# Optimization experiments

Hardware: AMD Instinct MI355X
Metric: run time of the kernel (lower is better)

## Reference

```python
import jax, jax.numpy as jnp
import numpy as np

B, C_IN, L, NCLASS = 256, 6, 512, 10

def setup_inputs() -> dict:
    key = jax.random.key(0)
    ks = jax.random.split(key, 16)
    g = lambda k, shp, s=0.05: jax.random.normal(k, shp, dtype=jnp.float32) * s
    return {
        "x": jax.random.normal(ks[0], (B, C_IN, L), dtype=jnp.float32),
        "conv1_w": g(ks[1], (32, C_IN, 3)),
        "conv1_b": g(ks[2], (32,)),
        "bn1_g": jnp.ones((32,), jnp.float32),
        "bn1_b": jnp.zeros((32,), jnp.float32),
        "bn1_m": g(ks[3], (32,)),
        "bn1_v": jnp.abs(g(ks[4], (32,))) + 1.0,
        "conv2_w": g(ks[5], (64, 32, 3)),
        "conv2_b": g(ks[6], (64,)),
        "bn2_g": jnp.ones((64,), jnp.float32),
        "bn2_b": jnp.zeros((64,), jnp.float32),
        "bn2_m": g(ks[7], (64,)),
        "bn2_v": jnp.abs(g(ks[8], (64,))) + 1.0,
        "wq": g(ks[9], (64, 64)),
        "bq": g(ks[10], (64,)),
        "wk": g(ks[11], (64, 64)),
        "bk": g(ks[12], (64,)),
        "wv": g(ks[13], (64, 64)),
        "bv": g(ks[14], (64,)),
        "fc_w": g(ks[15], (NCLASS, 64)),
        "fc_b": jnp.zeros((NCLASS,), jnp.float32),
    }

def _conv1d(x, w, b):
    # x: [B, C, L], w: [O, C, 3], padding=1 -> same length
    y = jax.lax.conv_general_dilated(
        x, w, window_strides=(1,), padding=[(1, 1)],
        dimension_numbers=("NCH", "OIH", "NCH"))
    return y + b[None, :, None]

def _bn(x, g, b, m, v, eps=1e-5):
    # eval-mode BatchNorm1d over channel dim of [B, C, L]
    inv = g * jax.lax.rsqrt(v + eps)
    return x * inv[None, :, None] + (b - m * inv)[None, :, None]

def reference(x, conv1_w, conv1_b, bn1_g, bn1_b, bn1_m, bn1_v,
              conv2_w, conv2_b, bn2_g, bn2_b, bn2_m, bn2_v,
              wq, bq, wk, bk, wv, bv, fc_w, fc_b):
    h = jax.nn.relu(_bn(_conv1d(x, conv1_w, conv1_b), bn1_g, bn1_b, bn1_m, bn1_v))
    h = jax.nn.relu(_bn(_conv1d(h, conv2_w, conv2_b), bn2_g, bn2_b, bn2_m, bn2_v))
    h = h.transpose(0, 2, 1)                      # [B, L, 64]
    q = h @ wq.T + bq
    k = h @ wk.T + bk
    v = h @ wv.T + bv
    scores = jnp.einsum("bqd,bkd->bqk", q, k) / jnp.sqrt(jnp.float32(64.0))
    attn = jax.nn.softmax(scores, axis=-1)
    out = jnp.einsum("bqk,bkd->bqd", attn, v)     # [B, L, 64]
    pooled = out.mean(axis=1)                     # [B, 64]
    return pooled @ fc_w.T + fc_b                 # [B, n_class]
```

## Files before the change

kernel.cpp:

```cpp
#include <hip/hip_runtime.h>
#include <hip/hip_bf16.h>


#define NB 256
#define LL 512
#define CIN 6
#define NCLASS 10
#define SLAB 9472
#define QSC 0.18033688f

typedef __bf16 bf16x8 __attribute__((ext_vector_type(8)));
typedef float f32x4 __attribute__((ext_vector_type(4)));
typedef unsigned short us4 __attribute__((ext_vector_type(4)));

static __device__ __forceinline__ unsigned short f2b(float f) {
    __bf16 h = (__bf16)f;
    return __builtin_bit_cast(unsigned short, h);
}

__global__ __launch_bounds__(256) void prep_weights(
    const float* __restrict__ w1, const float* __restrict__ cb1,
    const float* __restrict__ g1, const float* __restrict__ be1,
    const float* __restrict__ m1, const float* __restrict__ v1,
    const float* __restrict__ w2, const float* __restrict__ cb2,
    const float* __restrict__ g2, const float* __restrict__ be2,
    const float* __restrict__ m2, const float* __restrict__ v2,
    const float* __restrict__ wq, const float* __restrict__ wk,
    const float* __restrict__ wv,
    unsigned short* __restrict__ w1p, float* __restrict__ b1f,
    unsigned short* __restrict__ w2p, float* __restrict__ b2f,
    unsigned short* __restrict__ wqp, unsigned short* __restrict__ wkp,
    unsigned short* __restrict__ wvp)
{
    const int t = threadIdx.x;
    for (int idx = t; idx < 1024; idx += 256) {
        int c = idx >> 5, k = idx & 31;
        int dl = k >> 3, ci = k & 7;
        float inv = g1[c] * rsqrtf(v1[c] + 1e-5f);
        float val = (dl < 3 && ci < 6) ? w1[c * 18 + ci * 3 + dl] * inv : 0.f;
        w1p[idx] = f2b(val);
    }
    if (t < 32) {
        float inv = g1[t] * rsqrtf(v1[t] + 1e-5f);
        b1f[t] = be1[t] + (cb1[t] - m1[t]) * inv;
    }
    for (int idx = t; idx < 2048; idx += 256) {
        int c2 = idx >> 5, ci = idx & 31;
        float inv = g2[c2] * rsqrtf(v2[c2] + 1e-5f);
        const float* wp = w2 + c2 * 96 + ci * 3;
        w2p[c2 * 96 +      ci] = f2b(wp[0] * inv);
        w2p[c2 * 96 + 32 + ci] = f2b(wp[1] * inv);
        w2p[c2 * 96 + 64 + ci] = f2b(wp[2] * inv);
    }
    if (t >= 64 && t < 128) {
        int c2 = t - 64;
        float inv = g2[c2] * rsqrtf(v2[c2] + 1e-5f);
        b2f[c2] = be2[c2] + (cb2[c2] - m2[c2]) * inv;
    }
    for (int idx = t; idx < 4096; idx += 256) {
        wqp[idx] = f2b(wq[idx] * QSC);
        wkp[idx] = f2b(wk[idx]);
        wvp[idx] = f2b(wv[idx]);
    }
}

__global__ __launch_bounds__(1024, 4) void fused_all(
    const float* __restrict__ x,
    const unsigned short* __restrict__ w1p, const float* __restrict__ b1f,
    const unsigned short* __restrict__ w2p, const float* __restrict__ b2f,
    const unsigned short* __restrict__ wqp, const unsigned short* __restrict__ wkp,
    const unsigned short* __restrict__ wvp,
    const float* __restrict__ bq, const float* __restrict__ bk,
    const float* __restrict__ bvp,
    const float* __restrict__ fcw, const float* __restrict__ fcb,
    float* __restrict__ outp)
{
    const int b = blockIdx.x;
    const int t = threadIdx.x;
    const int w = t >> 6, lane = t & 63, quad = lane >> 4, lc = lane & 15;

    __shared__ __align__(16) char smem[16 * SLAB + 6144];
    char* myslab = smem + w * SLAB;
    unsigned short* h1sl = (unsigned short*)(myslab + 3072);
    unsigned short* Ts   = (unsigned short*)(myslab + 4608);
    unsigned short* Kf   = (unsigned short*)myslab;
    unsigned short* Vf   = (unsigned short*)(myslab + 4096);
    float* redw   = (float*)(myslab + 8192);
    float* pooled = (float*)(smem + 8448);
    unsigned short* xstage = (unsigned short*)(smem + 16 * SLAB);

    if (t < 768) {
        int ci = t >> 7, j4 = (t & 127) * 4;
        float4 xv = *(const float4*)(x + ((size_t)b * CIN + ci) * LL + j4);
        us4 pk;
        pk[0] = f2b(xv.x); pk[1] = f2b(xv.y); pk[2] = f2b(xv.z); pk[3] = f2b(xv.w);
        *(us4*)&xstage[ci * 512 + j4] = pk;
    }
    __syncthreads();

    bf16x8 bW1[2];
    #pragma unroll
    for (int nt = 0; nt < 2; nt++)
        bW1[nt] = *(const bf16x8*)(w1p + (nt * 16 + lc) * 32 + quad * 8);
    float b1v[2] = {b1f[lc], b1f[16 + lc]};
    f32x4 h1acc[3][2];
    #pragma unroll
    for (int mt = 0; mt < 3; mt++) {
        int pos = w * 32 - 2 + mt * 16 + lc + quad;
        bool ok = (quad < 3) && (pos >= 0) && (pos < LL);
        int posc = pos < 0 ? 0 : (pos > 511 ? 511 : pos);
        bf16x8 aX;
        #pragma unroll
        for (int u = 0; u < 6; u++) {
            __bf16 vb = __builtin_bit_cast(__bf16, xstage[u * 512 + posc]);
            aX[u] = ok ? vb : (__bf16)0.f;
        }
        aX[6] = (__bf16)0.f; aX[7] = (__bf16)0.f;
        #pragma unroll
        for (int nt = 0; nt < 2; nt++) {
            f32x4 z = {0.f, 0.f, 0.f, 0.f};
            h1acc[mt][nt] = __builtin_amdgcn_mfma_f32_16x16x32_bf16(aX, bW1[nt], z, 0, 0, 0);
        }
    }
    #pragma unroll
    for (int mt = 0; mt < 3; mt++)
        #pragma unroll
        for (int nt = 0; nt < 2; nt++)
            #pragma unroll
            for (int r = 0; r < 4; r++) {
                int j = mt * 16 + quad * 4 + r;
                if (j < 34) {
                    int pos = w * 32 - 1 + j;
                    float y = h1acc[mt][nt][r] + b1v[nt];
                    y = (pos >= 0 && pos < LL && y > 0.f) ? y : 0.f;
                    h1sl[j * 40 + nt * 16 + lc] = f2b(y);
                }
            }

    bf16x8 bX[2][3], aW2[4][3];
    #pragma unroll
    for (int rt = 0; rt < 2; rt++)
        #pragma unroll
        for (int kc = 0; kc < 3; kc++)
            bX[rt][kc] = *(const bf16x8*)&h1sl[(rt * 16 + lc + kc) * 40 + quad * 8];
    #pragma unroll
    for (int nt = 0; nt < 4; nt++)
        #pragma unroll
        for (int kc = 0; kc < 3; kc++)
            aW2[nt][kc] = *(const bf16x8*)(w2p + (nt * 16 + lc) * 96 + kc * 32 + quad * 8);

    f32x4 acc2[4][2];
    #pragma unroll
    for (int nt = 0; nt < 4; nt++)
        #pragma unroll
        for (int rt = 0; rt < 2; rt++) {
            f32x4 a = {0.f, 0.f, 0.f, 0.f};
            a = __builtin_amdgcn_mfma_f32_16x16x32_bf16(aW2[nt][0], bX[rt][0], a, 0, 0, 0);
            a = __builtin_amdgcn_mfma_f32_16x16x32_bf16(aW2[nt][1], bX[rt][1], a, 0, 0, 0);
            acc2[nt][rt] = __builtin_amdgcn_mfma_f32_16x16x32_bf16(aW2[nt][2], bX[rt][2], a, 0, 0, 0);
        }

    #pragma unroll
    for (int nt = 0; nt < 4; nt++) {
        const float4 bb2 = *(const float4*)&b2f[nt * 16 + quad * 4];
        #pragma unroll
        for (int rt = 0; rt < 2; rt++) {
            us4 pk;
            float y0 = acc2[nt][rt][0] + bb2.x; pk[0] = f2b(y0 > 0.f ? y0 : 0.f);
            float y1 = acc2[nt][rt][1] + bb2.y; pk[1] = f2b(y1 > 0.f ? y1 : 0.f);
            float y2 = acc2[nt][rt][2] + bb2.z; pk[2] = f2b(y2 > 0.f ? y2 : 0.f);
            float y3 = acc2[nt][rt][3] + bb2.w; pk[3] = f2b(y3 > 0.f ? y3 : 0.f);
            *(us4*)&Ts[(rt * 16 + lc) * 72 + nt * 16 + quad * 4] = pk;
        }
    }
    bf16x8 aH[2][2];
    #pragma unroll
    for (int rt = 0; rt < 2; rt++)
        #pragma unroll
        for (int kc = 0; kc < 2; kc++)
            aH[rt][kc] = *(const bf16x8*)&Ts[(rt * 16 + lc) * 72 + kc * 32 + quad * 8];

    bf16x8 aQ[2][2];
    for (int p = 0; p < 2; p++) {
        const unsigned short* wsrc = p ? wkp : wqp;
        const float* bsrc = p ? bk : bq;
        const float bscl = p ? 1.0f : QSC;
        #pragma unroll
        for (int nt = 0; nt < 4; nt++) {
            bf16x8 aW[2];
            #pragma unroll
            for (int kc = 0; kc < 2; kc++)
                aW[kc] = *(const bf16x8*)(wsrc + (nt * 16 + lc) * 64 + kc * 32 + quad * 8);
            float4 bb = *(const float4*)&bsrc[nt * 16 + quad * 4];
            bb.x *= bscl; bb.y *= bscl; bb.z *= bscl; bb.w *= bscl;
            #pragma unroll
            for (int rt = 0; rt < 2; rt++) {
                f32x4 a = {0.f, 0.f, 0.f, 0.f};
                a = __builtin_amdgcn_mfma_f32_16x16x32_bf16(aW[0], aH[rt][0], a, 0, 0, 0);
                a = __builtin_amdgcn_mfma_f32_16x16x32_bf16(aW[1], aH[rt][1], a, 0, 0, 0);
                us4 pk;
                pk[0] = f2b(a[0] + bb.x); pk[1] = f2b(a[1] + bb.y);
                pk[2] = f2b(a[2] + bb.z); pk[3] = f2b(a[3] + bb.w);
                *(us4*)&Ts[(rt * 16 + lc) * 72 + nt * 16 + quad * 4] = pk;
            }
        }
        #pragma unroll
        for (int rt = 0; rt < 2; rt++)
            #pragma unroll
            for (int kc = 0; kc < 2; kc++) {
                bf16x8 fr = *(const bf16x8*)&Ts[(rt * 16 + lc) * 72 + kc * 32 + quad * 8];
                if (p == 0) aQ[rt][kc] = fr;
                else *(bf16x8*)&Kf[((rt * 2 + kc) << 9) + lane * 8] = fr;
            }
    }

    #pragma unroll
    for (int nt = 0; nt < 4; nt++) {
        bf16x8 bW[2];
        #pragma unroll
        for (int kc = 0; kc < 2; kc++)
            bW[kc] = *(const bf16x8*)(wvp + (nt * 16 + lc) * 64 + kc * 32 + quad * 8);
        const float bvv = bvp[nt * 16 + lc];
        #pragma unroll
        for (int rt = 0; rt < 2; rt++) {
            f32x4 a = {0.f, 0.f, 0.f, 0.f};
            a = __builtin_amdgcn_mfma_f32_16x16x32_bf16(aH[rt][0], bW[0], a, 0, 0, 0);
            a = __builtin_amdgcn_mfma_f32_16x16x32_bf16(aH[rt][1], bW[1], a, 0, 0, 0);
            us4 pk;
            pk[0] = f2b(a[0] + bvv); pk[1] = f2b(a[1] + bvv);
            pk[2] = f2b(a[2] + bvv); pk[3] = f2b(a[3] + bvv);
            *(us4*)&Vf[nt * 512 + quad * 128 + lc * 8 + rt * 4] = pk;
        }
    }

    __syncthreads();

    f32x4 outacc[2][4];
    #pragma unroll
    for (int rt = 0; rt < 2; rt++)
        #pragma unroll
        for (int dt = 0; dt < 4; dt++) outacc[rt][dt] = (f32x4){0.f, 0.f, 0.f, 0.f};
    float den[2] = {0.f, 0.f};

    bf16x8 bK[2][2], bKn[2][2];
    {
        const unsigned short* sK = (const unsigned short*)smem;
        #pragma unroll
        for (int nt = 0; nt < 2; nt++)
            #pragma unroll
            for (int kc = 0; kc < 2; kc++)
                bK[nt][kc] = *(const bf16x8*)&sK[((nt * 2 + kc) << 9) + lane * 8];
    }

    for (int cc = 0; cc < 16; cc++) {
        f32x4 sv[2][2];
        #pragma unroll
        for (int nt = 0; nt < 2; nt++)
            #pragma unroll
            for (int rt = 0; rt < 2; rt++) {
                f32x4 z = {0.f, 0.f, 0.f, 0.f};
                z = __builtin_amdgcn_mfma_f32_16x16x32_bf16(bK[nt][0], aQ[rt][0], z, 0, 0, 0);
                sv[nt][rt] = __builtin_amdgcn_mfma_f32_16x16x32_bf16(bK[nt][1], aQ[rt][1], z, 0, 0, 0);
            }
        const unsigned short* sV = (const unsigned short*)(smem + cc * SLAB + 4096);
        bf16x8 bV[4];
        #pragma unroll
        for (int dt = 0; dt < 4; dt++)
            bV[dt] = *(const bf16x8*)&sV[dt * 512 + lane * 8];
        if (cc < 15) {
            const unsigned short* sKn = (const unsigned short*)(smem + (cc + 1) * SLAB);
            #pragma unroll
            for (int nt = 0; nt < 2; nt++)
                #pragma unroll
                for (int kc = 0; kc < 2; kc++)
                    bKn[nt][kc] = *(const bf16x8*)&sKn[((nt * 2 + kc) << 9) + lane * 8];
        }
        bf16x8 aP[2];
        #pragma unroll
        for (int rt = 0; rt < 2; rt++)
            #pragma unroll
            for (int nt = 0; nt < 2; nt++)
                #pragma unroll
                for (int reg = 0; reg < 4; reg++) {
                    float p = __builtin_amdgcn_exp2f(sv[nt][rt][reg]);
                    den[rt] += p;
                    aP[rt][nt * 4 + reg] = (__bf16)p;
                }
        #pragma unroll
        for (int dt = 0; dt < 4; dt++) {
            outacc[0][dt] = __builtin_amdgcn_mfma_f32_16x16x32_bf16(aP[0], bV[dt], outacc[0][dt], 0, 0, 0);
            outacc[1][dt] = __builtin_amdgcn_mfma_f32_16x16x32_bf16(aP[1], bV[dt], outacc[1][dt], 0, 0, 0);
        }
        #pragma unroll
        for (int nt = 0; nt < 2; nt++)
            #pragma unroll
            for (int kc = 0; kc < 2; kc++)
                bK[nt][kc] = bKn[nt][kc];
    }

    float rden[2][4];
    #pragma unroll
    for (int rt = 0; rt < 2; rt++) {
        float d2 = den[rt];
        d2 += __shfl_xor(d2, 16);
        d2 += __shfl_xor(d2, 32);
        d2 = 1.0f / d2;
        #pragma unroll
        for (int reg = 0; reg < 4; reg++)
            rden[rt][reg] = __shfl(d2, quad * 4 + reg);
    }
    #pragma unroll
    for (int dt = 0; dt < 4; dt++) {
        float ps = 0.f;
        #pragma unroll
        for (int rt = 0; rt < 2; rt++)
            #pragma unroll
            for (int reg = 0; reg < 4; reg++)
                ps += outacc[rt][dt][reg] * rden[rt][reg];
        ps += __shfl_xor(ps, 16);
        ps += __shfl_xor(ps, 32);
        if (quad == 0) redw[dt * 16 + lc] = ps;
    }
    __syncthreads();
    if (t < 64) {
        float s = 0.f;
        #pragma unroll
        for (int ww = 0; ww < 16; ww++)
            s += *(const float*)(smem + ww * SLAB + 8192 + t * 4);
        pooled[t] = s * (1.0f / 512.0f);
    }
    __syncthreads();
    if (t < NCLASS) {
        float acc = fcb[t];
        #pragma unroll
        for (int d = 0; d < 64; d++) acc += pooled[d] * fcw[t * 64 + d];
        outp[b * NCLASS + t] = acc;
    }
}

extern "C" void kernel_launch(void* const* d_in, const int* in_sizes, int n_in,
                              void* d_out, int out_size, void* d_ws, size_t ws_size,
                              hipStream_t stream)
{
    const float* x   = (const float*)d_in[0];
    const float* w1  = (const float*)d_in[1];
    const float* cb1 = (const float*)d_in[2];
    const float* g1  = (const float*)d_in[3];
    const float* be1 = (const float*)d_in[4];
    const float* m1  = (const float*)d_in[5];
    const float* v1  = (const float*)d_in[6];
    const float* w2  = (const float*)d_in[7];
    const float* cb2 = (const float*)d_in[8];
    const float* g2  = (const float*)d_in[9];
    const float* be2 = (const float*)d_in[10];
    const float* m2  = (const float*)d_in[11];
    const float* v2  = (const float*)d_in[12];
    const float* wq  = (const float*)d_in[13];
    const float* bq  = (const float*)d_in[14];
    const float* wk  = (const float*)d_in[15];
    const float* bk  = (const float*)d_in[16];
    const float* wv  = (const float*)d_in[17];
    const float* bv  = (const float*)d_in[18];
    const float* fcw = (const float*)d_in[19];
    const float* fcb = (const float*)d_in[20];
    float* out = (float*)d_out;

    char* ws = (char*)d_ws;
    unsigned short* w1p = (unsigned short*)(ws);
    float*          b1f = (float*)(ws + 2048u);
    float*          b2f = (float*)(ws + 2176u);
    unsigned short* w2p = (unsigned short*)(ws + 2432u);
    unsigned short* wqp = (unsigned short*)(ws + 14720u);
    unsigned short* wkp = (unsigned short*)(ws + 22912u);
    unsigned short* wvp = (unsigned short*)(ws + 31104u);

    prep_weights<<<dim3(1), 256, 0, stream>>>(w1, cb1, g1, be1, m1, v1,
                                              w2, cb2, g2, be2, m2, v2,
                                              wq, wk, wv,
                                              w1p, b1f, w2p, b2f, wqp, wkp, wvp);
    fused_all<<<dim3(NB), 1024, 0, stream>>>(x, w1p, b1f, w2p, b2f,
                                             wqp, wkp, wvp,
                                             bq, bk, bv, fcw, fcb, out);
}
```

Baseline: 130.8 us.

## Keep Q/K/H in registers via permuted weight layout and software-pipeline QK^T

Weights for Q/K/V are pre-permuted so MFMA output fragments map directly into the next MFMA's input layout, removing the LDS round-trips through the Ts scratch buffer. The per-wave slab is shrunk, x is staged position-major as 8-wide vectors so conv1 input is a single vector load, and conv1 results are written as packed vectors. The attention loop computes the next chunk's scores after the PV MFMAs under raised wave priority to overlap exp with matrix work. It adds register pressure and relies on an intricate channel permutation being correct.

```diff
diff --git a/kernel.cpp b/kernel.cpp
--- a/kernel.cpp
+++ b/kernel.cpp
@@ -6,12 +6,14 @@
 #define LL 512
 #define CIN 6
 #define NCLASS 10
-#define SLAB 9472
+#define SLAB 8192
 #define QSC 0.18033688f
 
 typedef __bf16 bf16x8 __attribute__((ext_vector_type(8)));
 typedef float f32x4 __attribute__((ext_vector_type(4)));
 typedef unsigned short us4 __attribute__((ext_vector_type(4)));
+typedef unsigned short us8 __attribute__((ext_vector_type(8)));
+typedef unsigned int u32x4 __attribute__((ext_vector_type(4)));
 
 static __device__ __forceinline__ unsigned short f2b(float f) {
     __bf16 h = (__bf16)f;
@@ -58,9 +60,12 @@
         b2f[c2] = be2[c2] + (cb2[c2] - m2[c2]) * inv;
     }
     for (int idx = t; idx < 4096; idx += 256) {
-        wqp[idx] = f2b(wq[idx] * QSC);
-        wkp[idx] = f2b(wk[idx]);
-        wvp[idx] = f2b(wv[idx]);
+        int d = idx >> 6, k = idx & 63;
+        int kc = k >> 5, quad = (k >> 3) & 3, e = k & 7;
+        int ch = kc * 32 + (e >> 2) * 16 + quad * 4 + (e & 3);
+        wqp[idx] = f2b(wq[d * 64 + ch] * QSC);
+        wkp[idx] = f2b(wk[d * 64 + ch]);
+        wvp[idx] = f2b(wv[d * 64 + ch]);
     }
 }
 
@@ -79,22 +84,22 @@
     const int t = threadIdx.x;
     const int w = t >> 6, lane = t & 63, quad = lane >> 4, lc = lane & 15;
 
-    __shared__ __align__(16) char smem[16 * SLAB + 6144];
+    __shared__ __align__(16) char smem[16 * SLAB + 8192];
     char* myslab = smem + w * SLAB;
-    unsigned short* h1sl = (unsigned short*)(myslab + 3072);
-    unsigned short* Ts   = (unsigned short*)(myslab + 4608);
+    unsigned short* h1sl = (unsigned short*)myslab;
     unsigned short* Kf   = (unsigned short*)myslab;
     unsigned short* Vf   = (unsigned short*)(myslab + 4096);
-    float* redw   = (float*)(myslab + 8192);
-    float* pooled = (float*)(smem + 8448);
     unsigned short* xstage = (unsigned short*)(smem + 16 * SLAB);
-
-    if (t < 768) {
-        int ci = t >> 7, j4 = (t & 127) * 4;
-        float4 xv = *(const float4*)(x + ((size_t)b * CIN + ci) * LL + j4);
-        us4 pk;
-        pk[0] = f2b(xv.x); pk[1] = f2b(xv.y); pk[2] = f2b(xv.z); pk[3] = f2b(xv.w);
-        *(us4*)&xstage[ci * 512 + j4] = pk;
+    float* redw   = (float*)(smem + 16 * SLAB) + w * 64;
+    float* pooled = (float*)(smem + 16 * SLAB + 4096);
+
+    if (t < 512) {
+        us8 pk;
+        #pragma unroll
+        for (int ci = 0; ci < 6; ci++)
+            pk[ci] = f2b(x[((size_t)b * CIN + ci) * LL + t]);
+        pk[6] = 0; pk[7] = 0;
+        *(us8*)&xstage[t * 8] = pk;
     }
     __syncthreads();
 
@@ -102,40 +107,36 @@
     #pragma unroll
     for (int nt = 0; nt < 2; nt++)
         bW1[nt] = *(const bf16x8*)(w1p + (nt * 16 + lc) * 32 + quad * 8);
-    float b1v[2] = {b1f[lc], b1f[16 + lc]};
-    f32x4 h1acc[3][2];
+    f32x4 b1q[2];
+    #pragma unroll
+    for (int nt = 0; nt < 2; nt++)
+        b1q[nt] = *(const f32x4*)&b1f[nt * 16 + quad * 4];
     #pragma unroll
     for (int mt = 0; mt < 3; mt++) {
-        int pos = w * 32 - 2 + mt * 16 + lc + quad;
-        bool ok = (quad < 3) && (pos >= 0) && (pos < LL);
-        int posc = pos < 0 ? 0 : (pos > 511 ? 511 : pos);
-        bf16x8 aX;
-        #pragma unroll
-        for (int u = 0; u < 6; u++) {
-            __bf16 vb = __builtin_bit_cast(__bf16, xstage[u * 512 + posc]);
-            aX[u] = ok ? vb : (__bf16)0.f;
-        }
-        aX[6] = (__bf16)0.f; aX[7] = (__bf16)0.f;
+        int j = mt * 16 + lc;
+        int P = w * 32 - 1 + j;
+        int src = P + quad - 1;
+        bool okx = (src >= 0) && (src < LL);
+        int srcc = src < 0 ? 0 : (src > 511 ? 511 : src);
+        u32x4 xv = *(const u32x4*)&xstage[srcc * 8];
+        if (!okx) { xv[0] = 0u; xv[1] = 0u; xv[2] = 0u; xv[3] = 0u; }
+        bf16x8 aX = __builtin_bit_cast(bf16x8, xv);
+        bool pv = (P >= 0) && (P < LL);
         #pragma unroll
         for (int nt = 0; nt < 2; nt++) {
             f32x4 z = {0.f, 0.f, 0.f, 0.f};
-            h1acc[mt][nt] = __builtin_amdgcn_mfma_f32_16x16x32_bf16(aX, bW1[nt], z, 0, 0, 0);
-        }
-    }
-    #pragma unroll
-    for (int mt = 0; mt < 3; mt++)
-        #pragma unroll
-        for (int nt = 0; nt < 2; nt++)
+            f32x4 h = __builtin_amdgcn_mfma_f32_16x16x32_bf16(bW1[nt], aX, z, 0, 0, 0);
+            us4 pk;
             #pragma unroll
             for (int r = 0; r < 4; r++) {
-                int j = mt * 16 + quad * 4 + r;
-                if (j < 34) {
-                    int pos = w * 32 - 1 + j;
-                    float y = h1acc[mt][nt][r] + b1v[nt];
-                    y = (pos >= 0 && pos < LL && y > 0.f) ? y : 0.f;
-                    h1sl[j * 40 + nt * 16 + lc] = f2b(y);
-                }
+                float y = h[r] + b1q[nt][r];
+                y = (pv && y > 0.f) ? y : 0.f;
+                pk[r] = f2b(y);
             }
+            if (j < 34)
+                *(us4*)&h1sl[j * 40 + nt * 16 + quad * 4] = pk;
+        }
+    }
 
     bf16x8 bX[2][3], aW2[4][3];
     #pragma unroll
@@ -160,77 +161,94 @@
             acc2[nt][rt] = __builtin_amdgcn_mfma_f32_16x16x32_bf16(aW2[nt][2], bX[rt][2], a, 0, 0, 0);
         }
 
-    #pragma unroll
-    for (int nt = 0; nt < 4; nt++) {
-        const float4 bb2 = *(const float4*)&b2f[nt * 16 + quad * 4];
-        #pragma unroll
-        for (int rt = 0; rt < 2; rt++) {
-            us4 pk;
-            float y0 = acc2[nt][rt][0] + bb2.x; pk[0] = f2b(y0 > 0.f ? y0 : 0.f);
-            float y1 = acc2[nt][rt][1] + bb2.y; pk[1] = f2b(y1 > 0.f ? y1 : 0.f);
-            float y2 = acc2[nt][rt][2] + bb2.z; pk[2] = f2b(y2 > 0.f ? y2 : 0.f);
-            float y3 = acc2[nt][rt][3] + bb2.w; pk[3] = f2b(y3 > 0.f ? y3 : 0.f);
-            *(us4*)&Ts[(rt * 16 + lc) * 72 + nt * 16 + quad * 4] = pk;
-        }
-    }
     bf16x8 aH[2][2];
     #pragma unroll
-    for (int rt = 0; rt < 2; rt++)
-        #pragma unroll
-        for (int kc = 0; kc < 2; kc++)
-            aH[rt][kc] = *(const bf16x8*)&Ts[(rt * 16 + lc) * 72 + kc * 32 + quad * 8];
+    for (int nt2 = 0; nt2 < 4; nt2++) {
+        f32x4 bb2 = *(const f32x4*)&b2f[nt2 * 16 + quad * 4];
+        #pragma unroll
+        for (int rt = 0; rt < 2; rt++)
+            #pragma unroll
+            for (int reg = 0; reg < 4; reg++) {
+                float y = acc2[nt2][rt][reg] + bb2[reg];
+                aH[rt][nt2 >> 1][(nt2 & 1) * 4 + reg] = (__bf16)(y > 0.f ? y : 0.f);
+            }
+    }
 
     bf16x8 aQ[2][2];
-    for (int p = 0; p < 2; p++) {
-        const unsigned short* wsrc = p ? wkp : wqp;
-        const float* bsrc = p ? bk : bq;
-        const float bscl = p ? 1.0f : QSC;
+    {
+        f32x4 Cq[4][2], bbq[4];
         #pragma unroll
         for (int nt = 0; nt < 4; nt++) {
-            bf16x8 aW[2];
-            #pragma unroll
-            for (int kc = 0; kc < 2; kc++)
-                aW[kc] = *(const bf16x8*)(wsrc + (nt * 16 + lc) * 64 + kc * 32 + quad * 8);
-            float4 bb = *(const float4*)&bsrc[nt * 16 + quad * 4];
-            bb.x *= bscl; bb.y *= bscl; bb.z *= bscl; bb.w *= bscl;
+            bf16x8 aW0 = *(const bf16x8*)(wqp + (nt * 16 + lc) * 64 + quad * 8);
+            bf16x8 aW1 = *(const bf16x8*)(wqp + (nt * 16 + lc) * 64 + 32 + quad * 8);
+            bbq[nt] = *(const f32x4*)&bq[nt * 16 + quad * 4];
             #pragma unroll
             for (int rt = 0; rt < 2; rt++) {
                 f32x4 a = {0.f, 0.f, 0.f, 0.f};
-                a = __builtin_amdgcn_mfma_f32_16x16x32_bf16(aW[0], aH[rt][0], a, 0, 0, 0);
-                a = __builtin_amdgcn_mfma_f32_16x16x32_bf16(aW[1], aH[rt][1], a, 0, 0, 0);
-                us4 pk;
-                pk[0] = f2b(a[0] + bb.x); pk[1] = f2b(a[1] + bb.y);
-                pk[2] = f2b(a[2] + bb.z); pk[3] = f2b(a[3] + bb.w);
-                *(us4*)&Ts[(rt * 16 + lc) * 72 + nt * 16 + quad * 4] = pk;
+                a = __builtin_amdgcn_mfma_f32_16x16x32_bf16(aW0, aH[rt][0], a, 0, 0, 0);
+                Cq[nt][rt] = __builtin_amdgcn_mfma_f32_16x16x32_bf16(aW1, aH[rt][1], a, 0, 0, 0);
             }
         }
         #pragma unroll
         for (int rt = 0; rt < 2; rt++)
             #pragma unroll
+            for (int nt = 0; nt < 4; nt++)
+                #pragma unroll
+                for (int reg = 0; reg < 4; reg++)
+                    aQ[rt][nt >> 1][(nt & 1) * 4 + reg] =
+                        (__bf16)(Cq[nt][rt][reg] + bbq[nt][reg] * QSC);
+    }
+    {
+        f32x4 Ck[4][2], bbk[4];
+        #pragma unroll
+        for (int nt = 0; nt < 4; nt++) {
+            bf16x8 aW0 = *(const bf16x8*)(wkp + (nt * 16 + lc) * 64 + quad * 8);
+            bf16x8 aW1 = *(const bf16x8*)(wkp + (nt * 16 + lc) * 64 + 32 + quad * 8);
+            bbk[nt] = *(const f32x4*)&bk[nt * 16 + quad * 4];
+            #pragma unroll
+            for (int rt = 0; rt < 2; rt++) {
+                f32x4 a = {0.f, 0.f, 0.f, 0.f};
+                a = __builtin_amdgcn_mfma_f32_16x16x32_bf16(aW0, aH[rt][0], a, 0, 0, 0);
+                Ck[nt][rt] = __builtin_amdgcn_mfma_f32_16x16x32_bf16(aW1, aH[rt][1], a, 0, 0, 0);
+            }
+        }
+        #pragma unroll
+        for (int rt = 0; rt < 2; rt++)
+            #pragma unroll
             for (int kc = 0; kc < 2; kc++) {
-                bf16x8 fr = *(const bf16x8*)&Ts[(rt * 16 + lc) * 72 + kc * 32 + quad * 8];
-                if (p == 0) aQ[rt][kc] = fr;
-                else *(bf16x8*)&Kf[((rt * 2 + kc) << 9) + lane * 8] = fr;
+                us8 pk;
+                #pragma unroll
+                for (int e = 0; e < 8; e++) {
+                    int nt = kc * 2 + (e >> 2), reg = e & 3;
+                    pk[e] = f2b(Ck[nt][rt][reg] + bbk[nt][reg]);
+                }
+                *(us8*)&Kf[((rt * 2 + kc) << 9) + lane * 8] = pk;
             }
     }
 
     #pragma unroll
     for (int nt = 0; nt < 4; nt++) {
-        bf16x8 bW[2];
-        #pragma unroll
-        for (int kc = 0; kc < 2; kc++)
-            bW[kc] = *(const bf16x8*)(wvp + (nt * 16 + lc) * 64 + kc * 32 + quad * 8);
+        bf16x8 bW0 = *(const bf16x8*)(wvp + (nt * 16 + lc) * 64 + quad * 8);
+        bf16x8 bW1 = *(const bf16x8*)(wvp + (nt * 16 + lc) * 64 + 32 + quad * 8);
         const float bvv = bvp[nt * 16 + lc];
-        #pragma unroll
-        for (int rt = 0; rt < 2; rt++) {
-            f32x4 a = {0.f, 0.f, 0.f, 0.f};
-            a = __builtin_amdgcn_mfma_f32_16x16x32_bf16(aH[rt][0], bW[0], a, 0, 0, 0);
-            a = __builtin_amdgcn_mfma_f32_16x16x32_bf16(aH[rt][1], bW[1], a, 0, 0, 0);
-            us4 pk;
-            pk[0] = f2b(a[0] + bvv); pk[1] = f2b(a[1] + bvv);
-            pk[2] = f2b(a[2] + bvv); pk[3] = f2b(a[3] + bvv);
-            *(us4*)&Vf[nt * 512 + quad * 128 + lc * 8 + rt * 4] = pk;
-        }
+        f32x4 a0, a1;
+        {
+            f32x4 z = {0.f, 0.f, 0.f, 0.f};
+            z = __builtin_amdgcn_mfma_f32_16x16x32_bf16(aH[0][0], bW0, z, 0, 0, 0);
+            a0 = __builtin_amdgcn_mfma_f32_16x16x32_bf16(aH[0][1], bW1, z, 0, 0, 0);
+        }
+        {
+            f32x4 z = {0.f, 0.f, 0.f, 0.f};
+            z = __builtin_amdgcn_mfma_f32_16x16x32_bf16(aH[1][0], bW0, z, 0, 0, 0);
+            a1 = __builtin_amdgcn_mfma_f32_16x16x32_bf16(aH[1][1], bW1, z, 0, 0, 0);
+        }
+        us8 pk;
+        #pragma unroll
+        for (int reg = 0; reg < 4; reg++) {
+            pk[reg]     = f2b(a0[reg] + bvv);
+            pk[4 + reg] = f2b(a1[reg] + bvv);
+        }
+        *(us8*)&Vf[nt * 512 + lane * 8] = pk;
     }
 
     __syncthreads();
@@ -242,26 +260,26 @@
         for (int dt = 0; dt < 4; dt++) outacc[rt][dt] = (f32x4){0.f, 0.f, 0.f, 0.f};
     float den[2] = {0.f, 0.f};
 
-    bf16x8 bK[2][2], bKn[2][2];
+    bf16x8 bK2[2][2];
     {
         const unsigned short* sK = (const unsigned short*)smem;
         #pragma unroll
         for (int nt = 0; nt < 2; nt++)
             #pragma unroll
             for (int kc = 0; kc < 2; kc++)
-                bK[nt][kc] = *(const bf16x8*)&sK[((nt * 2 + kc) << 9) + lane * 8];
-    }
+                bK2[nt][kc] = *(const bf16x8*)&sK[((nt * 2 + kc) << 9) + lane * 8];
+    }
+    f32x4 sv[2][2];
+    #pragma unroll
+    for (int nt = 0; nt < 2; nt++)
+        #pragma unroll
+        for (int rt = 0; rt < 2; rt++) {
+            f32x4 z = {0.f, 0.f, 0.f, 0.f};
+            z = __builtin_amdgcn_mfma_f32_16x16x32_bf16(bK2[nt][0], aQ[rt][0], z, 0, 0, 0);
+            sv[nt][rt] = __builtin_amdgcn_mfma_f32_16x16x32_bf16(bK2[nt][1], aQ[rt][1], z, 0, 0, 0);
+        }
 
     for (int cc = 0; cc < 16; cc++) {
-        f32x4 sv[2][2];
-        #pragma unroll
-        for (int nt = 0; nt < 2; nt++)
-            #pragma unroll
-            for (int rt = 0; rt < 2; rt++) {
-                f32x4 z = {0.f, 0.f, 0.f, 0.f};
-                z = __builtin_amdgcn_mfma_f32_16x16x32_bf16(bK[nt][0], aQ[rt][0], z, 0, 0, 0);
-                sv[nt][rt] = __builtin_amdgcn_mfma_f32_16x16x32_bf16(bK[nt][1], aQ[rt][1], z, 0, 0, 0);
-            }
         const unsigned short* sV = (const unsigned short*)(smem + cc * SLAB + 4096);
         bf16x8 bV[4];
         #pragma unroll
@@ -273,7 +291,7 @@
             for (int nt = 0; nt < 2; nt++)
                 #pragma unroll
                 for (int kc = 0; kc < 2; kc++)
-                    bKn[nt][kc] = *(const bf16x8*)&sKn[((nt * 2 + kc) << 9) + lane * 8];
+                    bK2[nt][kc] = *(const bf16x8*)&sKn[((nt * 2 + kc) << 9) + lane * 8];
         }
         bf16x8 aP[2];
         #pragma unroll
@@ -286,16 +304,23 @@
                     den[rt] += p;
                     aP[rt][nt * 4 + reg] = (__bf16)p;
                 }
+        __builtin_amdgcn_s_setprio(1);
         #pragma unroll
         for (int dt = 0; dt < 4; dt++) {
             outacc[0][dt] = __builtin_amdgcn_mfma_f32_16x16x32_bf16(aP[0], bV[dt], outacc[0][dt], 0, 0, 0);
             outacc[1][dt] = __builtin_amdgcn_mfma_f32_16x16x32_bf16(aP[1], bV[dt], outacc[1][dt], 0, 0, 0);
         }
-        #pragma unroll
-        for (int nt = 0; nt < 2; nt++)
-            #pragma unroll
-            for (int kc = 0; kc < 2; kc++)
-                bK[nt][kc] = bKn[nt][kc];
+        if (cc < 15) {
+            #pragma unroll
+            for (int nt = 0; nt < 2; nt++)
+                #pragma unroll
+                for (int rt = 0; rt < 2; rt++) {
+                    f32x4 z = {0.f, 0.f, 0.f, 0.f};
+                    z = __builtin_amdgcn_mfma_f32_16x16x32_bf16(bK2[nt][0], aQ[rt][0], z, 0, 0, 0);
+                    sv[nt][rt] = __builtin_amdgcn_mfma_f32_16x16x32_bf16(bK2[nt][1], aQ[rt][1], z, 0, 0, 0);
+                }
+        }
+        __builtin_amdgcn_s_setprio(0);
     }
 
     float rden[2][4];
@@ -326,7 +351,7 @@
         float s = 0.f;
         #pragma unroll
         for (int ww = 0; ww < 16; ww++)
-            s += *(const float*)(smem + ww * SLAB + 8192 + t * 4);
+            s += *(const float*)(smem + 16 * SLAB + ww * 256 + t * 4);
         pooled[t] = s * (1.0f / 512.0f);
     }
     __syncthreads();
```

New measurement: 130.0 us. No clear change (-0.6%).
